# Performance work log

Hardware: AMD Instinct MI355X
Metric: run time of the kernel (lower is better)

The kernel has to match this reference:

```python
import jax, jax.numpy as jnp
import numpy as np

B, T, D, U = 64, 512, 1024, 128


def setup_inputs() -> dict:
    key = jax.random.key(0)
    k1, k2, k3, k4, k5 = jax.random.split(key, 5)
    x = jax.random.normal(k1, (B, T, D), dtype=jnp.float32)
    mask = jnp.ones((B, T), dtype=jnp.int32)
    # learned parameters (glorot-ish scale for kernel)
    kernel = jax.random.normal(k2, (D, U), dtype=jnp.float32) * (1.0 / np.sqrt(D))
    bias = jnp.zeros((U,), dtype=jnp.float32)
    left_boundary = jax.random.normal(k3, (U,), dtype=jnp.float32) * 0.1
    right_boundary = jax.random.normal(k4, (U,), dtype=jnp.float32) * 0.1
    return {"x": x, "mask": mask, "kernel": kernel, "bias": bias,
            "left_boundary": left_boundary, "right_boundary": right_boundary}


def _shift_right(m):  # [B,T,1] -> pad one zero step at front along time
    return jnp.concatenate([jnp.zeros_like(m[:, :1]), m[:, :-1]], axis=1)


def _shift_left(m):  # [B,T,1] -> pad one zero step at end along time
    return jnp.concatenate([m[:, 1:], jnp.zeros_like(m[:, :1])], axis=1)


def reference(x, mask, kernel, bias, left_boundary, right_boundary):
    # input energy: linear activation of dense projection  [B,T,U]
    energy = jnp.einsum('btd,du->btu', x, kernel) + bias
    # boundary energies with mask (faithful to source semantics)
    m = mask.astype(energy.dtype)[:, :, None]                     # [B,T,1]
    start_mask = (m > _shift_right(m)).astype(energy.dtype)       # first valid step
    end_mask = (_shift_left(m) > m).astype(energy.dtype)          # as written in source
    energy = energy + start_mask * left_boundary[None, None, :]
    energy = energy + end_mask * right_boundary[None, None, :]
    return energy
```

## Files before the change

kernel.cpp:

```cpp
#include <hip/hip_runtime.h>

#define TT 512
#define DD 1024
#define UU 128
#define MM 32768
#define BK 64
#define NCHUNK 16

typedef short short8 __attribute__((ext_vector_type(8)));
typedef float f32x4 __attribute__((ext_vector_type(4)));

__device__ __forceinline__ unsigned short f2bf(float f) {
    union { float f; unsigned u; } v; v.f = f;
    unsigned u = v.u;
    return (unsigned short)((u + 0x7fffu + ((u >> 16) & 1u)) >> 16);
}

__device__ __forceinline__ void glds16(const void* g, void* l) {
    __builtin_amdgcn_global_load_lds(
        (const __attribute__((address_space(1))) void*)g,
        (__attribute__((address_space(3))) void*)l, 16, 0, 0);
}

__global__ __launch_bounds__(256) void wprep_kernel(const float* __restrict__ w,
                                                    unsigned short* __restrict__ wt) {
    int tg = blockIdx.x * 256 + threadIdx.x;
    int kg = tg & 7;
    int n  = (tg >> 3) & 127;
    int kc = tg >> 10;
    union { unsigned short s[8]; uint4 v; } o;
#pragma unroll
    for (int j = 0; j < 8; ++j) {
        int k = kc * 64 + kg * 8 + j;
        o.s[j] = f2bf(w[k * 128 + n]);
    }
    *(uint4*)(wt + tg * 8) = o.v;
}

__global__ __launch_bounds__(256, 2) void crf_energy_kernel(
    const float* __restrict__ x,
    const int* __restrict__ mask,
    const unsigned short* __restrict__ wt,
    const float* __restrict__ bias,
    const float* __restrict__ lb,
    const float* __restrict__ rb,
    float* __restrict__ out)
{
    __shared__ float lAf[2][64 * 64];
    __shared__ unsigned short lBs[2][128 * 64];

    const int tid  = threadIdx.x;
    const int w    = tid >> 6;
    const int lane = tid & 63;
    const int q    = lane >> 4;
    const int r    = lane & 15;

    const int mh   = w >> 1;
    const int nh   = w & 1;
    const int row0 = blockIdx.x * 64;

    int a_m[4], a_g[4];
#pragma unroll
    for (int j = 0; j < 4; ++j) {
        a_m[j] = w * 16 + j * 4 + (lane >> 4);
        a_g[j] = (lane & 15) ^ (a_m[j] & 15);
    }
    int b_n[4], b_g[4];
#pragma unroll
    for (int j = 0; j < 4; ++j) {
        b_n[j] = w * 32 + j * 8 + (lane >> 3);
        b_g[j] = (lane & 7) ^ (b_n[j] & 7);
    }

    f32x4 acc[2][4];
#pragma unroll
    for (int mt = 0; mt < 2; ++mt)
#pragma unroll
        for (int nt = 0; nt < 4; ++nt) acc[mt][nt] = (f32x4){0.f, 0.f, 0.f, 0.f};

#pragma unroll
    for (int j = 0; j < 4; ++j)
        glds16(x + (size_t)(row0 + a_m[j]) * DD + a_g[j] * 4,
               (char*)lAf[0] + w * 4096 + j * 1024);
#pragma unroll
    for (int j = 0; j < 4; ++j)
        glds16(wt + b_n[j] * 64 + b_g[j] * 8,
               (char*)lBs[0] + w * 4096 + j * 1024);
    __syncthreads();

    for (int kc = 0; kc < NCHUNK; ++kc) {
        const int cb = kc & 1;

        if (kc < NCHUNK - 1) {
            const int pb = cb ^ 1;
#pragma unroll
            for (int j = 0; j < 4; ++j)
                glds16(x + (size_t)(row0 + a_m[j]) * DD + (kc + 1) * BK + a_g[j] * 4,
                       (char*)lAf[pb] + w * 4096 + j * 1024);
#pragma unroll
            for (int j = 0; j < 4; ++j)
                glds16(wt + (size_t)(kc + 1) * 8192 + b_n[j] * 64 + b_g[j] * 8,
                       (char*)lBs[pb] + w * 4096 + j * 1024);
        }

        const float* const lA = lAf[cb];
        const unsigned short* const lB = lBs[cb];
#pragma unroll
        for (int ks = 0; ks < 2; ++ks) {
            short8 a[2];
#pragma unroll
            for (int mt = 0; mt < 2; ++mt) {
                const int m  = mh * 32 + mt * 16 + r;
                const int g0 = ks * 8 + q * 2;
                const float4 lo = *(const float4*)(&lA[m * 64 + (((g0    ) ^ (m & 15)) * 4)]);
                const float4 hi = *(const float4*)(&lA[m * 64 + (((g0 + 1) ^ (m & 15)) * 4)]);
                union { unsigned short s[8]; short8 v; } pk;
                pk.s[0] = f2bf(lo.x); pk.s[1] = f2bf(lo.y);
                pk.s[2] = f2bf(lo.z); pk.s[3] = f2bf(lo.w);
                pk.s[4] = f2bf(hi.x); pk.s[5] = f2bf(hi.y);
                pk.s[6] = f2bf(hi.z); pk.s[7] = f2bf(hi.w);
                a[mt] = pk.v;
            }
            short8 b[4];
            const int gb = ks * 4 + q;
#pragma unroll
            for (int nt = 0; nt < 4; ++nt) {
                const int n = nh * 64 + nt * 16 + r;
                b[nt] = *(const short8*)(&lB[n * 64 + ((gb ^ (n & 7)) * 8)]);
            }
#pragma unroll
            for (int mt = 0; mt < 2; ++mt)
#pragma unroll
                for (int nt = 0; nt < 4; ++nt)
                    acc[mt][nt] = __builtin_amdgcn_mfma_f32_16x16x32_bf16(
                        a[mt], b[nt], acc[mt][nt], 0, 0, 0);
        }

        __syncthreads();
    }

#pragma unroll
    for (int mt = 0; mt < 2; ++mt) {
#pragma unroll
        for (int reg = 0; reg < 4; ++reg) {
            const int m = row0 + mh * 32 + mt * 16 + q * 4 + reg;
            const int t = m & (TT - 1);
            const int cur  = mask[m];
            const int prev = (t != 0)      ? mask[m - 1] : 0;
            const int nxt  = (t != TT - 1) ? mask[m + 1] : 0;
            const float sm = (cur > prev) ? 1.f : 0.f;
            const float em = (nxt > cur)  ? 1.f : 0.f;
#pragma unroll
            for (int nt = 0; nt < 4; ++nt) {
                const int n = nh * 64 + nt * 16 + r;
                float e = acc[mt][nt][reg] + bias[n] + sm * lb[n] + em * rb[n];
                out[(size_t)m * UU + n] = e;
            }
        }
    }
}

extern "C" void kernel_launch(void* const* d_in, const int* in_sizes, int n_in,
                              void* d_out, int out_size, void* d_ws, size_t ws_size,
                              hipStream_t stream) {
    const float* x    = (const float*)d_in[0];
    const int*   mask = (const int*)d_in[1];
    const float* w    = (const float*)d_in[2];
    const float* bias = (const float*)d_in[3];
    const float* lb   = (const float*)d_in[4];
    const float* rb   = (const float*)d_in[5];
    float* out = (float*)d_out;
    unsigned short* wt = (unsigned short*)d_ws;

    wprep_kernel<<<64, 256, 0, stream>>>(w, wt);
    crf_energy_kernel<<<512, 256, 0, stream>>>(x, mask, wt, bias, lb, rb, out);
}
```

Baseline: 214.0 us.

## Deepen GEMM K-pipeline to four LDS stages with vmcnt waits and packed bf16 convert

Halves the K chunk to 32, keeps four LDS buffers with three loads in flight, and replaces the per-chunk __syncthreads with an explicit vmcnt wait plus barrier, so global-to-LDS loads overlap MFMA work across several iterations. The weight prep layout changes to match the 32-wide chunks. Software round-to-nearest bf16 packing is replaced by the hardware v_cvt_pk_bf16_f32 instruction. The cost is twice as many barriers per K, less work per chunk, and correctness depends on the hand-written vmcnt counts.

```diff
diff --git a/kernel.cpp b/kernel.cpp
--- a/kernel.cpp
+++ b/kernel.cpp
@@ -4,8 +4,8 @@
 #define DD 1024
 #define UU 128
 #define MM 32768
-#define BK 64
-#define NCHUNK 16
+#define BK 32
+#define NCHUNK 32
 
 typedef short short8 __attribute__((ext_vector_type(8)));
 typedef float f32x4 __attribute__((ext_vector_type(4)));
@@ -14,6 +14,15 @@
     union { float f; unsigned u; } v; v.f = f;
     unsigned u = v.u;
     return (unsigned short)((u + 0x7fffu + ((u >> 16) & 1u)) >> 16);
+}
+
+__device__ __forceinline__ short8 cvt8(float4 lo, float4 hi) {
+    union { unsigned u[4]; short8 v; } o;
+    asm("v_cvt_pk_bf16_f32 %0, %1, %2" : "=v"(o.u[0]) : "v"(lo.x), "v"(lo.y));
+    asm("v_cvt_pk_bf16_f32 %0, %1, %2" : "=v"(o.u[1]) : "v"(lo.z), "v"(lo.w));
+    asm("v_cvt_pk_bf16_f32 %0, %1, %2" : "=v"(o.u[2]) : "v"(hi.x), "v"(hi.y));
+    asm("v_cvt_pk_bf16_f32 %0, %1, %2" : "=v"(o.u[3]) : "v"(hi.z), "v"(hi.w));
+    return o.v;
 }
 
 __device__ __forceinline__ void glds16(const void* g, void* l) {
@@ -25,16 +34,16 @@
 __global__ __launch_bounds__(256) void wprep_kernel(const float* __restrict__ w,
                                                     unsigned short* __restrict__ wt) {
     int tg = blockIdx.x * 256 + threadIdx.x;
-    int kg = tg & 7;
-    int n  = (tg >> 3) & 127;
-    int kc = tg >> 10;
+    int n  = tg & 127;
+    int kg = (tg >> 7) & 3;
+    int kc = tg >> 9;
     union { unsigned short s[8]; uint4 v; } o;
 #pragma unroll
     for (int j = 0; j < 8; ++j) {
-        int k = kc * 64 + kg * 8 + j;
+        int k = kc * 32 + kg * 8 + j;
         o.s[j] = f2bf(w[k * 128 + n]);
     }
-    *(uint4*)(wt + tg * 8) = o.v;
+    *(uint4*)(wt + kc * 4096 + n * 32 + kg * 8) = o.v;
 }
 
 __global__ __launch_bounds__(256, 2) void crf_energy_kernel(
@@ -46,8 +55,8 @@
     const float* __restrict__ rb,
     float* __restrict__ out)
 {
-    __shared__ float lAf[2][64 * 64];
-    __shared__ unsigned short lBs[2][128 * 64];
+    __shared__ float lAf[4][64 * 32];
+    __shared__ unsigned short lBs[4][128 * 32];
 
     const int tid  = threadIdx.x;
     const int w    = tid >> 6;
@@ -59,17 +68,17 @@
     const int nh   = w & 1;
     const int row0 = blockIdx.x * 64;
 
-    int a_m[4], a_g[4];
+    int a_m[2], a_g[2];
 #pragma unroll
-    for (int j = 0; j < 4; ++j) {
-        a_m[j] = w * 16 + j * 4 + (lane >> 4);
-        a_g[j] = (lane & 15) ^ (a_m[j] & 15);
+    for (int j = 0; j < 2; ++j) {
+        a_m[j] = w * 16 + j * 8 + (lane >> 3);
+        a_g[j] = (lane & 7) ^ (a_m[j] & 7);
     }
-    int b_n[4], b_g[4];
+    int b_n[2], b_g[2];
 #pragma unroll
-    for (int j = 0; j < 4; ++j) {
-        b_n[j] = w * 32 + j * 8 + (lane >> 3);
-        b_g[j] = (lane & 7) ^ (b_n[j] & 7);
+    for (int j = 0; j < 2; ++j) {
+        b_n[j] = w * 32 + j * 16 + (lane >> 2);
+        b_g[j] = (lane & 3) ^ (b_n[j] & 3);
     }
 
     f32x4 acc[2][4];
@@ -78,66 +87,65 @@
 #pragma unroll
         for (int nt = 0; nt < 4; ++nt) acc[mt][nt] = (f32x4){0.f, 0.f, 0.f, 0.f};
 
-#pragma unroll
-    for (int j = 0; j < 4; ++j)
-        glds16(x + (size_t)(row0 + a_m[j]) * DD + a_g[j] * 4,
-               (char*)lAf[0] + w * 4096 + j * 1024);
-#pragma unroll
-    for (int j = 0; j < 4; ++j)
-        glds16(wt + b_n[j] * 64 + b_g[j] * 8,
-               (char*)lBs[0] + w * 4096 + j * 1024);
-    __syncthreads();
+#define STAGE(kc, bi) do {                                                      \
+    _Pragma("unroll")                                                           \
+    for (int j = 0; j < 2; ++j)                                                 \
+        glds16(x + (size_t)(row0 + a_m[j]) * DD + (kc) * BK + a_g[j] * 4,       \
+               (char*)lAf[bi] + w * 2048 + j * 1024);                           \
+    _Pragma("unroll")                                                           \
+    for (int j = 0; j < 2; ++j)                                                 \
+        glds16(wt + (kc) * 4096 + b_n[j] * 32 + b_g[j] * 8,                     \
+               (char*)lBs[bi] + w * 2048 + j * 1024);                           \
+} while (0)
 
-    for (int kc = 0; kc < NCHUNK; ++kc) {
-        const int cb = kc & 1;
+#define COMPUTE(bi) do {                                                        \
+    const float* lA = lAf[bi];                                                  \
+    const unsigned short* lB = lBs[bi];                                         \
+    short8 a[2];                                                                \
+    _Pragma("unroll")                                                           \
+    for (int mt = 0; mt < 2; ++mt) {                                            \
+        const int m  = mh * 32 + mt * 16 + r;                                   \
+        const int g0 = (2 * q)     ^ (m & 7);                                   \
+        const int g1 = (2 * q + 1) ^ (m & 7);                                   \
+        const float4 lo = *(const float4*)(&lA[m * 32 + g0 * 4]);               \
+        const float4 hi = *(const float4*)(&lA[m * 32 + g1 * 4]);               \
+        a[mt] = cvt8(lo, hi);                                                   \
+    }                                                                           \
+    short8 b[4];                                                                \
+    _Pragma("unroll")                                                           \
+    for (int nt = 0; nt < 4; ++nt) {                                            \
+        const int n = nh * 64 + nt * 16 + r;                                    \
+        b[nt] = *(const short8*)(&lB[n * 32 + ((q ^ (n & 3)) * 8)]);            \
+    }                                                                           \
+    _Pragma("unroll")                                                           \
+    for (int mt = 0; mt < 2; ++mt)                                              \
+        _Pragma("unroll")                                                       \
+        for (int nt = 0; nt < 4; ++nt)                                          \
+            acc[mt][nt] = __builtin_amdgcn_mfma_f32_16x16x32_bf16(              \
+                a[mt], b[nt], acc[mt][nt], 0, 0, 0);                            \
+} while (0)
 
-        if (kc < NCHUNK - 1) {
-            const int pb = cb ^ 1;
-#pragma unroll
-            for (int j = 0; j < 4; ++j)
-                glds16(x + (size_t)(row0 + a_m[j]) * DD + (kc + 1) * BK + a_g[j] * 4,
-                       (char*)lAf[pb] + w * 4096 + j * 1024);
-#pragma unroll
-            for (int j = 0; j < 4; ++j)
-                glds16(wt + (size_t)(kc + 1) * 8192 + b_n[j] * 64 + b_g[j] * 8,
-                       (char*)lBs[pb] + w * 4096 + j * 1024);
-        }
+#define WAITBAR(vstr) do {                                                      \
+    asm volatile("s_waitcnt vmcnt(" vstr ")" ::: "memory");                     \
+    __builtin_amdgcn_s_barrier();                                               \
+    __builtin_amdgcn_sched_barrier(0);                                          \
+} while (0)
 
-        const float* const lA = lAf[cb];
-        const unsigned short* const lB = lBs[cb];
-#pragma unroll
-        for (int ks = 0; ks < 2; ++ks) {
-            short8 a[2];
-#pragma unroll
-            for (int mt = 0; mt < 2; ++mt) {
-                const int m  = mh * 32 + mt * 16 + r;
-                const int g0 = ks * 8 + q * 2;
-                const float4 lo = *(const float4*)(&lA[m * 64 + (((g0    ) ^ (m & 15)) * 4)]);
-                const float4 hi = *(const float4*)(&lA[m * 64 + (((g0 + 1) ^ (m & 15)) * 4)]);
-                union { unsigned short s[8]; short8 v; } pk;
-                pk.s[0] = f2bf(lo.x); pk.s[1] = f2bf(lo.y);
-                pk.s[2] = f2bf(lo.z); pk.s[3] = f2bf(lo.w);
-                pk.s[4] = f2bf(hi.x); pk.s[5] = f2bf(hi.y);
-                pk.s[6] = f2bf(hi.z); pk.s[7] = f2bf(hi.w);
-                a[mt] = pk.v;
-            }
-            short8 b[4];
-            const int gb = ks * 4 + q;
-#pragma unroll
-            for (int nt = 0; nt < 4; ++nt) {
-                const int n = nh * 64 + nt * 16 + r;
-                b[nt] = *(const short8*)(&lB[n * 64 + ((gb ^ (n & 7)) * 8)]);
-            }
-#pragma unroll
-            for (int mt = 0; mt < 2; ++mt)
-#pragma unroll
-                for (int nt = 0; nt < 4; ++nt)
-                    acc[mt][nt] = __builtin_amdgcn_mfma_f32_16x16x32_bf16(
-                        a[mt], b[nt], acc[mt][nt], 0, 0, 0);
-        }
+    STAGE(0, 0);
+    STAGE(1, 1);
+    STAGE(2, 2);
 
-        __syncthreads();
+    for (int kc = 0; kc < NCHUNK - 3; ++kc) {
+        WAITBAR("8");
+        STAGE(kc + 3, (kc + 3) & 3);
+        COMPUTE(kc & 3);
     }
+    WAITBAR("8");
+    COMPUTE(1);
+    WAITBAR("4");
+    COMPUTE(2);
+    WAITBAR("0");
+    COMPUTE(3);
 
 #pragma unroll
     for (int mt = 0; mt < 2; ++mt) {
@@ -158,6 +166,9 @@
             }
         }
     }
+#undef STAGE
+#undef COMPUTE
+#undef WAITBAR
 }
 
 extern "C" void kernel_launch(void* const* d_in, const int* in_sizes, int n_in,
```

Measured after the change: 215.4 us. Within noise of the previous version (+0.7%).
